# Optimization experiments

Hardware: AMD Instinct MI355X
Metric: run time of the kernel (lower is better)

The kernel has to match this reference:

```python
import jax, jax.numpy as jnp
import numpy as np

N = 100000        # nodes
E = 1600000       # edges (before self-loops)
IN_CH = 256       # input features
HEADS = 8         # conv1 heads; per-head dim also 8 (GATConv(in, heads, heads=heads))
HID = 8
NCLASS = 64
SLOPE = 0.2       # PyG leaky_relu negative slope


def _gat_conv(x, edge_index, W, att_src, att_dst, bias, heads, ch, concat):
    """PyG GATConv (eval mode): gather -> leaky_relu score -> segment softmax -> scatter."""
    n = x.shape[0]
    src, dst = edge_index[0], edge_index[1]
    h = (x @ W).reshape(n, heads, ch)                      # [N, H, C]
    a_src = jnp.einsum('nhc,hc->nh', h, att_src)           # [N, H]
    a_dst = jnp.einsum('nhc,hc->nh', h, att_dst)
    alpha = jax.nn.leaky_relu(a_src[src] + a_dst[dst], SLOPE)  # [E, H]
    # segment softmax over destination node
    amax = jax.ops.segment_max(alpha, dst, num_segments=n)     # [N, H]
    ex = jnp.exp(alpha - amax[dst])
    denom = jax.ops.segment_sum(ex, dst, num_segments=n)
    coef = ex / (denom[dst] + 1e-16)                           # [E, H]
    out = jax.ops.segment_sum(coef[:, :, None] * h[src], dst, num_segments=n)  # [N, H, C]
    if concat:
        out = out.reshape(n, heads * ch)
    else:
        out = out.mean(axis=1)
    return out + bias


def _add_self_loops(edge_index, n):
    loop = jnp.arange(n, dtype=edge_index.dtype)
    return jnp.concatenate([edge_index, jnp.stack([loop, loop])], axis=1)


def setup_inputs() -> dict:
    key = jax.random.key(0)
    ks = jax.random.split(key, 10)
    g = lambda k, shp, s: (jax.random.normal(k, shp, jnp.float32) * s)
    return {
        'x': jax.random.normal(ks[0], (N, IN_CH), jnp.float32),
        'edge_index': jax.random.randint(ks[1], (2, E), 0, N, dtype=jnp.int64),
        'W1': g(ks[2], (IN_CH, HEADS * HID), 1.0 / np.sqrt(IN_CH)),
        'att_src1': g(ks[3], (HEADS, HID), 0.3),
        'att_dst1': g(ks[4], (HEADS, HID), 0.3),
        'b1': jnp.zeros((HEADS * HID,), jnp.float32),
        'W2': g(ks[5], (HEADS * HID, NCLASS), 1.0 / np.sqrt(HEADS * HID)),
        'att_src2': g(ks[6], (1, NCLASS), 0.3),
        'att_dst2': g(ks[7], (1, NCLASS), 0.3),
        'b2': jnp.zeros((NCLASS,), jnp.float32),
    }


def reference(x, edge_index, W1, att_src1, att_dst1, b1, W2, att_src2, att_dst2, b2):
    ei = _add_self_loops(edge_index, x.shape[0])
    h = jax.nn.elu(_gat_conv(x, ei, W1, att_src1, att_dst1, b1, HEADS, HID, True))
    # dropout is a no-op in eval mode
    h = _gat_conv(h, ei, W2, att_src2, att_dst2, b2, 1, NCLASS, False)
    return jax.nn.log_softmax(h, axis=-1)
```

## Files before the change

### kernel.cpp

```cpp
#include <hip/hip_runtime.h>
#include <hip/hip_bf16.h>

#define LRELU_SLOPE 0.2f
#define CH2 6144
#define NBUK 256
#define BCAP 9728

typedef unsigned int uint;
typedef unsigned short ushort;
typedef short bt8 __attribute__((ext_vector_type(8)));
typedef float fx4 __attribute__((ext_vector_type(4)));

__device__ __forceinline__ float lrelu(float a) {
    return a > 0.f ? a : LRELU_SLOPE * a;
}
__device__ __forceinline__ ushort f2bf(float f) {
    uint u = __float_as_uint(f);
    return (ushort)((u + 0x7FFF + ((u >> 16) & 1)) >> 16);
}
__device__ __forceinline__ float bf2f(ushort h) {
    return __uint_as_float(((uint)h) << 16);
}

__global__ __launch_bounds__(256) void prep_wt(
    const float* __restrict__ W1, const float* __restrict__ W2,
    ushort* __restrict__ WT1, ushort* __restrict__ WT2)
{
    int idx = blockIdx.x * 256 + threadIdx.x;
    if (idx < 64 * 256) {
        int c = idx >> 8, k = idx & 255;
        WT1[idx] = f2bf(W1[k * 64 + c]);
    }
    int i2 = idx - 64 * 256;
    if (i2 >= 0 && i2 < 64 * 64) {
        int c = i2 >> 6, k = i2 & 63;
        WT2[i2] = f2bf(W2[k * 64 + c]);
    }
}

template<int K, bool INF32>
__global__ __launch_bounds__(256) void gemm_mfma(
    const void* __restrict__ Xv, const ushort* __restrict__ WT,
    ushort* __restrict__ OUT, int nrows)
{
    constexpr int LDW = K + 8;
    __shared__ ushort wt_l[64 * LDW];
    __shared__ ushort a_l[64 * 40];
    const int t = threadIdx.x;
    const int base = blockIdx.x * 64;

    for (int idx = t * 8; idx < 64 * K; idx += 256 * 8) {
        int r = idx / K, c = idx % K;
        *(uint4*)&wt_l[r * LDW + c] = *(const uint4*)&WT[idx];
    }
    __syncthreads();

    const int w = t >> 6, l = t & 63;
    const int frow = l & 15;
    const int kof = (l >> 4) * 8;
    fx4 acc[4] = {};

    for (int k0 = 0; k0 < K; k0 += 32) {
        if constexpr (INF32) {
            const float* X = (const float*)Xv;
            #pragma unroll
            for (int half = 0; half < 2; ++half) {
                int r = (t >> 3) + 32 * half;
                int kq = (t & 7) * 4;
                int gr = base + r;
                float4 v = make_float4(0.f, 0.f, 0.f, 0.f);
                if (gr < nrows) v = *(const float4*)(X + (size_t)gr * K + k0 + kq);
                ushort4 o;
                o.x = f2bf(v.x); o.y = f2bf(v.y); o.z = f2bf(v.z); o.w = f2bf(v.w);
                *(ushort4*)&a_l[r * 40 + kq] = o;
            }
        } else {
            const ushort* X = (const ushort*)Xv;
            int r = t >> 2;
            int kq = (t & 3) * 8;
            int gr = base + r;
            uint4 v = make_uint4(0, 0, 0, 0);
            if (gr < nrows) v = *(const uint4*)(X + (size_t)gr * K + k0 + kq);
            *(uint4*)&a_l[r * 40 + kq] = v;
        }
        __syncthreads();
        bt8 af = *(const bt8*)&a_l[(16 * w + frow) * 40 + kof];
        #pragma unroll
        for (int g = 0; g < 4; ++g) {
            bt8 bf = *(const bt8*)&wt_l[(16 * g + frow) * LDW + k0 + kof];
            acc[g] = __builtin_amdgcn_mfma_f32_16x16x32_bf16(af, bf, acc[g], 0, 0, 0);
        }
        __syncthreads();
    }

    const int orow0 = base + 16 * w + (l >> 4) * 4;
    const int ocol = l & 15;
    #pragma unroll
    for (int g = 0; g < 4; ++g) {
        #pragma unroll
        for (int r4 = 0; r4 < 4; ++r4) {
            int gr = orow0 + r4;
            if (gr < nrows) OUT[(size_t)gr * 64 + 16 * g + ocol] = f2bf(acc[g][r4]);
        }
    }
}

__global__ __launch_bounds__(256) void node_att_h8(
    const ushort* __restrict__ H, const float* __restrict__ att_s,
    const float* __restrict__ att_d,
    float* __restrict__ a_src, float* __restrict__ a_dst, int n)
{
    int node = blockIdx.x * 4 + (threadIdx.x >> 6);
    if (node >= n) return;
    int lane = threadIdx.x & 63;
    float h = bf2f(H[(size_t)node * 64 + lane]);
    float ps = h * att_s[lane];
    float pd = h * att_d[lane];
    #pragma unroll
    for (int off = 1; off < 8; off <<= 1) {
        ps += __shfl_xor(ps, off, 64);
        pd += __shfl_xor(pd, off, 64);
    }
    if ((lane & 7) == 0) {
        a_src[(size_t)node * 8 + (lane >> 3)] = ps;
        a_dst[(size_t)node * 8 + (lane >> 3)] = pd;
    }
}

__global__ __launch_bounds__(256) void node_att_h1(
    const ushort* __restrict__ H, const float* __restrict__ att_s,
    const float* __restrict__ att_d,
    float* __restrict__ a_src, float* __restrict__ a_dst, int n)
{
    int node = blockIdx.x * 4 + (threadIdx.x >> 6);
    if (node >= n) return;
    int lane = threadIdx.x & 63;
    float h = bf2f(H[(size_t)node * 64 + lane]);
    float ps = h * att_s[lane];
    float pd = h * att_d[lane];
    #pragma unroll
    for (int off = 1; off < 64; off <<= 1) {
        ps += __shfl_xor(ps, off, 64);
        pd += __shfl_xor(pd, off, 64);
    }
    if (lane == 0) { a_src[node] = ps; a_dst[node] = pd; }
}

__global__ void init_pcur(int* __restrict__ pcur)
{
    int t = threadIdx.x;
    if (t < NBUK) pcur[t] = t * BCAP;
}

__global__ __launch_bounds__(1024) void partition_pairs(
    const int* __restrict__ ei, int E_, int ET,
    int* __restrict__ pcur, uint* __restrict__ pairs)
{
    __shared__ int lcnt[NBUK], lsc[NBUK], lplace[NBUK], gpos[NBUK];
    const int t = threadIdx.x;
    const int base = blockIdx.x * CH2;
    const int total = min(CH2, ET - base);
    if (total <= 0) return;

    if (t < NBUK) lcnt[t] = 0;
    __syncthreads();

    uint pp[6]; int pk[6];
    #pragma unroll
    for (int i = 0; i < 6; ++i) {
        int idx = t + i * 1024;
        pk[i] = -1;
        if (idx < total) {
            int e = base + idx;
            int s, d;
            if (e < E_) { s = ei[e]; d = ei[E_ + e]; } else { s = d = e - E_; }
            pk[i] = d >> 9;
            pp[i] = (uint)s | ((uint)(d & 511) << 17);
            atomicAdd(&lcnt[pk[i]], 1);
        }
    }
    __syncthreads();

    if (t < NBUK) lsc[t] = lcnt[t];
    __syncthreads();
    for (int off = 1; off < NBUK; off <<= 1) {
        int add = 0;
        if (t < NBUK && t >= off) add = lsc[t - off];
        __syncthreads();
        if (t < NBUK) lsc[t] += add;
        __syncthreads();
    }
    if (t < NBUK) {
        int excl = lsc[t] - lcnt[t];
        lplace[t] = excl;
        int c = lcnt[t];
        gpos[t] = c ? (atomicAdd(&pcur[t], c) - excl) : 0;
    }
    __syncthreads();

    #pragma unroll
    for (int i = 0; i < 6; ++i) {
        if (pk[i] >= 0) {
            int slot = atomicAdd(&lplace[pk[i]], 1);
            pairs[gpos[pk[i]] + slot] = pp[i];
        }
    }
}

__global__ __launch_bounds__(256) void bucket_scan(
    const int* __restrict__ pcur, int* __restrict__ boff, int nbuk_used)
{
    __shared__ int sm[NBUK];
    int t = threadIdx.x;
    int v = (t < nbuk_used) ? (pcur[t] - t * BCAP) : 0;
    sm[t] = v; __syncthreads();
    for (int off = 1; off < NBUK; off <<= 1) {
        int add = (t >= off) ? sm[t - off] : 0;
        __syncthreads();
        sm[t] += add;
        __syncthreads();
    }
    boff[t] = sm[t] - v;
}

__global__ __launch_bounds__(1024) void phase2_build(
    const uint* __restrict__ pairs, const int* __restrict__ pcur,
    const int* __restrict__ boff,
    int* __restrict__ rp, int* __restrict__ ssrc, int n)
{
    __shared__ int hist[512], cur[512];
    const int k = blockIdx.x;
    const int t = threadIdx.x;
    const int beg = k * BCAP;
    const int cnt = pcur[k] - beg;
    const int bbase = boff[k];
    const int dbase = k << 9;

    if (t < 512) hist[t] = 0;
    __syncthreads();

    for (int i = t; i < cnt; i += 1024)
        atomicAdd(&hist[pairs[beg + i] >> 17], 1);
    __syncthreads();

    int c0 = (t < 512) ? hist[t] : 0;
    for (int off = 1; off < 512; off <<= 1) {
        int add = 0;
        if (t < 512 && t >= off) add = hist[t - off];
        __syncthreads();
        if (t < 512) hist[t] += add;
        __syncthreads();
    }
    if (t < 512) {
        int node = dbase + t;
        if (node < n) rp[node] = bbase + hist[t];
        cur[t] = hist[t] - c0;
    }
    __syncthreads();

    for (int i = t; i < cnt; i += 1024) {
        uint p = pairs[beg + i];
        int j = p >> 17;
        int pos = bbase + atomicAdd(&cur[j], 1);
        ssrc[pos] = (int)(p & 0x1FFFF);
    }
}

__global__ __launch_bounds__(256) void gather_h8(
    const int* __restrict__ rp, const int* __restrict__ ssrc,
    const float* __restrict__ a_src, const float* __restrict__ a_dst,
    const ushort* __restrict__ HB, const float* __restrict__ bias,
    ushort* __restrict__ HACT, int n)
{
    int node = blockIdx.x * 32 + (threadIdx.x >> 3);
    if (node >= n) return;
    int ol = threadIdx.x & 7;
    int end = rp[node];
    int start = node ? rp[node - 1] : 0;
    float adh = a_dst[(size_t)node * 8 + ol];
    float acc[8] = {};
    float dsum = 0.f;

    for (int i0 = start; i0 < end; i0 += 8) {
        int cnt = min(8, end - i0);
        int sv = (ol < cnt) ? ssrc[i0 + ol] : 0;
        #pragma unroll
        for (int j = 0; j < 8; ++j) {
            int sj = __shfl(sv, j, 8);
            float a = a_src[(size_t)sj * 8 + ol] + adh;
            a = a > 0.f ? a : LRELU_SLOPE * a;
            float e = __expf(a);
            e = (j < cnt) ? e : 0.f;
            dsum += e;
            uint4 hv = *(const uint4*)(HB + (size_t)sj * 64 + ol * 8);
            acc[0] += e * bf2f((ushort)(hv.x & 0xffff));
            acc[1] += e * bf2f((ushort)(hv.x >> 16));
            acc[2] += e * bf2f((ushort)(hv.y & 0xffff));
            acc[3] += e * bf2f((ushort)(hv.y >> 16));
            acc[4] += e * bf2f((ushort)(hv.z & 0xffff));
            acc[5] += e * bf2f((ushort)(hv.z >> 16));
            acc[6] += e * bf2f((ushort)(hv.w & 0xffff));
            acc[7] += e * bf2f((ushort)(hv.w >> 16));
        }
    }
    float inv = 1.f / (dsum + 1e-16f);
    float4 b0 = *(const float4*)(bias + ol * 8);
    float4 b1 = *(const float4*)(bias + ol * 8 + 4);
    float v[8];
    v[0] = acc[0] * inv + b0.x; v[1] = acc[1] * inv + b0.y;
    v[2] = acc[2] * inv + b0.z; v[3] = acc[3] * inv + b0.w;
    v[4] = acc[4] * inv + b1.x; v[5] = acc[5] * inv + b1.y;
    v[6] = acc[6] * inv + b1.z; v[7] = acc[7] * inv + b1.w;
    #pragma unroll
    for (int c = 0; c < 8; ++c) v[c] = v[c] > 0.f ? v[c] : expm1f(v[c]);
    uint4 o;
    o.x = (uint)f2bf(v[0]) | ((uint)f2bf(v[1]) << 16);
    o.y = (uint)f2bf(v[2]) | ((uint)f2bf(v[3]) << 16);
    o.z = (uint)f2bf(v[4]) | ((uint)f2bf(v[5]) << 16);
    o.w = (uint)f2bf(v[6]) | ((uint)f2bf(v[7]) << 16);
    *(uint4*)(HACT + (size_t)node * 64 + ol * 8) = o;
}

__global__ __launch_bounds__(256) void gather_h1_lsm(
    const int* __restrict__ rp, const int* __restrict__ ssrc,
    const float* __restrict__ a_src, const float* __restrict__ a_dst,
    const ushort* __restrict__ HB, const float* __restrict__ bias,
    float* __restrict__ OUT, int n)
{
    int node = blockIdx.x * 32 + (threadIdx.x >> 3);
    if (node >= n) return;
    int ol = threadIdx.x & 7;
    int end = rp[node];
    int start = node ? rp[node - 1] : 0;
    float ad = a_dst[node];
    float acc[8] = {};
    float dsum = 0.f;

    for (int i0 = start; i0 < end; i0 += 8) {
        int cnt = min(8, end - i0);
        int sv = (ol < cnt) ? ssrc[i0 + ol] : 0;
        #pragma unroll
        for (int j = 0; j < 8; ++j) {
            int sj = __shfl(sv, j, 8);
            float a = a_src[sj] + ad;
            a = a > 0.f ? a : LRELU_SLOPE * a;
            float e = __expf(a);
            e = (j < cnt) ? e : 0.f;
            dsum += e;
            uint4 hv = *(const uint4*)(HB + (size_t)sj * 64 + ol * 8);
            acc[0] += e * bf2f((ushort)(hv.x & 0xffff));
            acc[1] += e * bf2f((ushort)(hv.x >> 16));
            acc[2] += e * bf2f((ushort)(hv.y & 0xffff));
            acc[3] += e * bf2f((ushort)(hv.y >> 16));
            acc[4] += e * bf2f((ushort)(hv.z & 0xffff));
            acc[5] += e * bf2f((ushort)(hv.z >> 16));
            acc[6] += e * bf2f((ushort)(hv.w & 0xffff));
            acc[7] += e * bf2f((ushort)(hv.w >> 16));
        }
    }
    float inv = 1.f / (dsum + 1e-16f);
    float4 b0 = *(const float4*)(bias + ol * 8);
    float4 b1 = *(const float4*)(bias + ol * 8 + 4);
    float v[8];
    v[0] = acc[0] * inv + b0.x; v[1] = acc[1] * inv + b0.y;
    v[2] = acc[2] * inv + b0.z; v[3] = acc[3] * inv + b0.w;
    v[4] = acc[4] * inv + b1.x; v[5] = acc[5] * inv + b1.y;
    v[6] = acc[6] * inv + b1.z; v[7] = acc[7] * inv + b1.w;

    float m = v[0];
    #pragma unroll
    for (int c = 1; c < 8; ++c) m = fmaxf(m, v[c]);
    m = fmaxf(m, __shfl_xor(m, 1, 8));
    m = fmaxf(m, __shfl_xor(m, 2, 8));
    m = fmaxf(m, __shfl_xor(m, 4, 8));
    float s = 0.f;
    #pragma unroll
    for (int c = 0; c < 8; ++c) s += __expf(v[c] - m);
    s += __shfl_xor(s, 1, 8);
    s += __shfl_xor(s, 2, 8);
    s += __shfl_xor(s, 4, 8);
    float lse = m + __logf(s);
    float4 o0 = make_float4(v[0] - lse, v[1] - lse, v[2] - lse, v[3] - lse);
    float4 o1 = make_float4(v[4] - lse, v[5] - lse, v[6] - lse, v[7] - lse);
    *(float4*)(OUT + (size_t)node * 64 + ol * 8) = o0;
    *(float4*)(OUT + (size_t)node * 64 + ol * 8 + 4) = o1;
}

extern "C" void kernel_launch(void* const* d_in, const int* in_sizes, int n_in,
                              void* d_out, int out_size, void* d_ws, size_t ws_size,
                              hipStream_t stream)
{
    const float* x    = (const float*)d_in[0];
    const int*   ei   = (const int*)d_in[1];
    const float* W1   = (const float*)d_in[2];
    const float* as1w = (const float*)d_in[3];
    const float* ad1w = (const float*)d_in[4];
    const float* b1   = (const float*)d_in[5];
    const float* W2   = (const float*)d_in[6];
    const float* as2w = (const float*)d_in[7];
    const float* ad2w = (const float*)d_in[8];
    const float* b2   = (const float*)d_in[9];
    float* out = (float*)d_out;

    const int n  = in_sizes[0] / 256;
    const int E_ = in_sizes[1] / 2;
    const int ET = E_ + n;
    const int NBUKU = (n + 511) >> 9;

    char* wsb = (char*)d_ws;
    ushort* HACT = (ushort*)wsb;
    uint*   pairs= (uint*)wsb;
    ushort* HB   = HACT + (size_t)n * 64;
    float*  a_s1 = (float*)(HB + (size_t)n * 64);
    float*  a_d1 = a_s1 + (size_t)n * 8;
    float*  a_s2 = a_d1 + (size_t)n * 8;
    float*  a_d2 = a_s2 + n;
    int*    rp   = (int*)(a_d2 + n);
    int*    pcur = rp + n;
    int*    boff = pcur + NBUK;
    int*    ssrc = boff + NBUK;
    ushort* WT1  = (ushort*)(ssrc + ET);
    ushort* WT2  = WT1 + 64 * 256;

    const int gemm_grid = (n + 63) / 64;
    const int natt_grid = (n + 3) / 4;
    const int gath_grid = (n + 31) / 32;
    const int part_grid = (ET + CH2 - 1) / CH2;

    prep_wt<<<80, 256, 0, stream>>>(W1, W2, WT1, WT2);
    init_pcur<<<1, NBUK, 0, stream>>>(pcur);
    partition_pairs<<<part_grid, 1024, 0, stream>>>(ei, E_, ET, pcur, pairs);
    bucket_scan<<<1, NBUK, 0, stream>>>(pcur, boff, NBUKU);
    phase2_build<<<NBUKU, 1024, 0, stream>>>(pairs, pcur, boff, rp, ssrc, n);

    gemm_mfma<256, true><<<gemm_grid, 256, 0, stream>>>(x, WT1, HB, n);
    node_att_h8<<<natt_grid, 256, 0, stream>>>(HB, as1w, ad1w, a_s1, a_d1, n);
    gather_h8<<<gath_grid, 256, 0, stream>>>(rp, ssrc, a_s1, a_d1, HB, b1, HACT, n);

    gemm_mfma<64, false><<<gemm_grid, 256, 0, stream>>>(HACT, WT2, HB, n);
    node_att_h1<<<natt_grid, 256, 0, stream>>>(HB, as2w, ad2w, a_s2, a_d2, n);
    gather_h1_lsm<<<gath_grid, 256, 0, stream>>>(rp, ssrc, a_s2, a_d2, HB, b2, out, n);
}
```

Measured before the change: 189.6 us.

## Fuse partition with GEMM1, attention into GEMM epilogue, bucket scan into build

Several kernels are merged. Edge partitioning and the first GEMM now run as a single heterogeneous launch at 256-thread blocks over smaller chunks. The per-node attention dot products move into the GEMM epilogue using warp shuffles, the bucket scan is folded into phase2_build, and pcur init is folded into weight prep. The GEMM now reads weights directly from global memory instead of staging them in LDS, and the gather loops process 16 edges per iteration to expose more memory parallelism. The aim is fewer launches and fewer HB re-reads, at the cost of uncached weight reads and a redundant scan in every build block.

```diff
diff --git a/kernel.cpp b/kernel.cpp
--- a/kernel.cpp
+++ b/kernel.cpp
@@ -2,18 +2,15 @@
 #include <hip/hip_bf16.h>
 
 #define LRELU_SLOPE 0.2f
-#define CH2 6144
 #define NBUK 256
 #define BCAP 9728
+#define CH1 1536
 
 typedef unsigned int uint;
 typedef unsigned short ushort;
 typedef short bt8 __attribute__((ext_vector_type(8)));
 typedef float fx4 __attribute__((ext_vector_type(4)));
 
-__device__ __forceinline__ float lrelu(float a) {
-    return a > 0.f ? a : LRELU_SLOPE * a;
-}
 __device__ __forceinline__ ushort f2bf(float f) {
     uint u = __float_as_uint(f);
     return (ushort)((u + 0x7FFF + ((u >> 16) & 1)) >> 16);
@@ -22,11 +19,23 @@
     return __uint_as_float(((uint)h) << 16);
 }
 
-__global__ __launch_bounds__(256) void prep_wt(
+#define ACC8(e, hv) \
+    acc[0] += (e) * bf2f((ushort)((hv).x & 0xffff)); \
+    acc[1] += (e) * bf2f((ushort)((hv).x >> 16));    \
+    acc[2] += (e) * bf2f((ushort)((hv).y & 0xffff)); \
+    acc[3] += (e) * bf2f((ushort)((hv).y >> 16));    \
+    acc[4] += (e) * bf2f((ushort)((hv).z & 0xffff)); \
+    acc[5] += (e) * bf2f((ushort)((hv).z >> 16));    \
+    acc[6] += (e) * bf2f((ushort)((hv).w & 0xffff)); \
+    acc[7] += (e) * bf2f((ushort)((hv).w >> 16));
+
+__global__ __launch_bounds__(256) void prep_init(
     const float* __restrict__ W1, const float* __restrict__ W2,
-    ushort* __restrict__ WT1, ushort* __restrict__ WT2)
-{
-    int idx = blockIdx.x * 256 + threadIdx.x;
+    ushort* __restrict__ WT1, ushort* __restrict__ WT2, int* __restrict__ pcur)
+{
+    int t = threadIdx.x;
+    int idx = blockIdx.x * 256 + t;
+    if (blockIdx.x == 0) pcur[t] = t * BCAP;
     if (idx < 64 * 256) {
         int c = idx >> 8, k = idx & 255;
         WT1[idx] = f2bf(W1[k * 64 + c]);
@@ -38,23 +47,69 @@
     }
 }
 
-template<int K, bool INF32>
-__global__ __launch_bounds__(256) void gemm_mfma(
-    const void* __restrict__ Xv, const ushort* __restrict__ WT,
-    ushort* __restrict__ OUT, int nrows)
-{
-    constexpr int LDW = K + 8;
-    __shared__ ushort wt_l[64 * LDW];
-    __shared__ ushort a_l[64 * 40];
+__device__ __forceinline__ void partition_body(
+    int bid, const int* __restrict__ ei, int E_, int ET,
+    int* __restrict__ pcur, uint* __restrict__ pairs,
+    int* lcnt, int* lsc, int* lplace, int* gpos)
+{
     const int t = threadIdx.x;
-    const int base = blockIdx.x * 64;
-
-    for (int idx = t * 8; idx < 64 * K; idx += 256 * 8) {
-        int r = idx / K, c = idx % K;
-        *(uint4*)&wt_l[r * LDW + c] = *(const uint4*)&WT[idx];
-    }
-    __syncthreads();
-
+    const int base = bid * CH1;
+    const int total = min(CH1, ET - base);
+    if (total <= 0) return;
+
+    lcnt[t] = 0;
+    __syncthreads();
+
+    uint pp[6]; int pk[6];
+    #pragma unroll
+    for (int i = 0; i < 6; ++i) {
+        int idx = t + i * 256;
+        pk[i] = -1;
+        if (idx < total) {
+            int e = base + idx;
+            int s, d;
+            if (e < E_) { s = ei[e]; d = ei[E_ + e]; } else { s = d = e - E_; }
+            pk[i] = d >> 9;
+            pp[i] = (uint)s | ((uint)(d & 511) << 17);
+            atomicAdd(&lcnt[pk[i]], 1);
+        }
+    }
+    __syncthreads();
+
+    lsc[t] = lcnt[t];
+    __syncthreads();
+    for (int off = 1; off < NBUK; off <<= 1) {
+        int add = (t >= off) ? lsc[t - off] : 0;
+        __syncthreads();
+        lsc[t] += add;
+        __syncthreads();
+    }
+    {
+        int excl = lsc[t] - lcnt[t];
+        lplace[t] = excl;
+        int c = lcnt[t];
+        gpos[t] = c ? (atomicAdd(&pcur[t], c) - excl) : 0;
+    }
+    __syncthreads();
+
+    #pragma unroll
+    for (int i = 0; i < 6; ++i) {
+        if (pk[i] >= 0) {
+            int slot = atomicAdd(&lplace[pk[i]], 1);
+            pairs[gpos[pk[i]] + slot] = pp[i];
+        }
+    }
+}
+
+template<int K, bool INF32, int HEADS>
+__device__ __forceinline__ void gemm_body(
+    int bid, const void* __restrict__ Xv, const ushort* __restrict__ WT,
+    ushort* __restrict__ OUT, float* __restrict__ a_src, float* __restrict__ a_dst,
+    const float* __restrict__ att_s, const float* __restrict__ att_d,
+    int nrows, ushort* a_l)
+{
+    const int t = threadIdx.x;
+    const int base = bid * 64;
     const int w = t >> 6, l = t & 63;
     const int frow = l & 15;
     const int kof = (l >> 4) * 8;
@@ -76,8 +131,7 @@
             }
         } else {
             const ushort* X = (const ushort*)Xv;
-            int r = t >> 2;
-            int kq = (t & 3) * 8;
+            int r = t >> 2, kq = (t & 3) * 8;
             int gr = base + r;
             uint4 v = make_uint4(0, 0, 0, 0);
             if (gr < nrows) v = *(const uint4*)(X + (size_t)gr * K + k0 + kq);
@@ -87,7 +141,7 @@
         bt8 af = *(const bt8*)&a_l[(16 * w + frow) * 40 + kof];
         #pragma unroll
         for (int g = 0; g < 4; ++g) {
-            bt8 bf = *(const bt8*)&wt_l[(16 * g + frow) * LDW + k0 + kof];
+            bt8 bf = *(const bt8*)&WT[(size_t)(16 * g + frow) * K + k0 + kof];
             acc[g] = __builtin_amdgcn_mfma_f32_16x16x32_bf16(af, bf, acc[g], 0, 0, 0);
         }
         __syncthreads();
@@ -103,141 +157,99 @@
             if (gr < nrows) OUT[(size_t)gr * 64 + 16 * g + ocol] = f2bf(acc[g][r4]);
         }
     }
-}
-
-__global__ __launch_bounds__(256) void node_att_h8(
-    const ushort* __restrict__ H, const float* __restrict__ att_s,
-    const float* __restrict__ att_d,
-    float* __restrict__ a_src, float* __restrict__ a_dst, int n)
-{
-    int node = blockIdx.x * 4 + (threadIdx.x >> 6);
-    if (node >= n) return;
-    int lane = threadIdx.x & 63;
-    float h = bf2f(H[(size_t)node * 64 + lane]);
-    float ps = h * att_s[lane];
-    float pd = h * att_d[lane];
-    #pragma unroll
-    for (int off = 1; off < 8; off <<= 1) {
-        ps += __shfl_xor(ps, off, 64);
-        pd += __shfl_xor(pd, off, 64);
-    }
-    if ((lane & 7) == 0) {
-        a_src[(size_t)node * 8 + (lane >> 3)] = ps;
-        a_dst[(size_t)node * 8 + (lane >> 3)] = pd;
-    }
-}
-
-__global__ __launch_bounds__(256) void node_att_h1(
-    const ushort* __restrict__ H, const float* __restrict__ att_s,
-    const float* __restrict__ att_d,
-    float* __restrict__ a_src, float* __restrict__ a_dst, int n)
-{
-    int node = blockIdx.x * 4 + (threadIdx.x >> 6);
-    if (node >= n) return;
-    int lane = threadIdx.x & 63;
-    float h = bf2f(H[(size_t)node * 64 + lane]);
-    float ps = h * att_s[lane];
-    float pd = h * att_d[lane];
-    #pragma unroll
-    for (int off = 1; off < 64; off <<= 1) {
-        ps += __shfl_xor(ps, off, 64);
-        pd += __shfl_xor(pd, off, 64);
-    }
-    if (lane == 0) { a_src[node] = ps; a_dst[node] = pd; }
-}
-
-__global__ void init_pcur(int* __restrict__ pcur)
-{
-    int t = threadIdx.x;
-    if (t < NBUK) pcur[t] = t * BCAP;
-}
-
-__global__ __launch_bounds__(1024) void partition_pairs(
-    const int* __restrict__ ei, int E_, int ET,
-    int* __restrict__ pcur, uint* __restrict__ pairs)
+
+    float as_c[4], ad_c[4];
+    #pragma unroll
+    for (int g = 0; g < 4; ++g) {
+        as_c[g] = att_s[16 * g + ocol];
+        ad_c[g] = att_d[16 * g + ocol];
+    }
+    if constexpr (HEADS == 8) {
+        #pragma unroll
+        for (int r4 = 0; r4 < 4; ++r4) {
+            int gr = orow0 + r4;
+            #pragma unroll
+            for (int g = 0; g < 4; ++g) {
+                float ps = acc[g][r4] * as_c[g];
+                float pd = acc[g][r4] * ad_c[g];
+                ps += __shfl_xor(ps, 1, 64); pd += __shfl_xor(pd, 1, 64);
+                ps += __shfl_xor(ps, 2, 64); pd += __shfl_xor(pd, 2, 64);
+                ps += __shfl_xor(ps, 4, 64); pd += __shfl_xor(pd, 4, 64);
+                if ((l & 7) == 0 && gr < nrows) {
+                    int head = 2 * g + ((l >> 3) & 1);
+                    a_src[(size_t)gr * 8 + head] = ps;
+                    a_dst[(size_t)gr * 8 + head] = pd;
+                }
+            }
+        }
+    } else {
+        #pragma unroll
+        for (int r4 = 0; r4 < 4; ++r4) {
+            int gr = orow0 + r4;
+            float ps = 0.f, pd = 0.f;
+            #pragma unroll
+            for (int g = 0; g < 4; ++g) {
+                ps += acc[g][r4] * as_c[g];
+                pd += acc[g][r4] * ad_c[g];
+            }
+            ps += __shfl_xor(ps, 1, 64); pd += __shfl_xor(pd, 1, 64);
+            ps += __shfl_xor(ps, 2, 64); pd += __shfl_xor(pd, 2, 64);
+            ps += __shfl_xor(ps, 4, 64); pd += __shfl_xor(pd, 4, 64);
+            ps += __shfl_xor(ps, 8, 64); pd += __shfl_xor(pd, 8, 64);
+            if ((l & 15) == 0 && gr < nrows) {
+                a_src[gr] = ps;
+                a_dst[gr] = pd;
+            }
+        }
+    }
+}
+
+__global__ __launch_bounds__(256) void part_gemm1(
+    const int* __restrict__ ei, int E_, int ET, int part_grid,
+    int* __restrict__ pcur, uint* __restrict__ pairs,
+    const float* __restrict__ x, const ushort* __restrict__ WT1,
+    ushort* __restrict__ HB, float* __restrict__ a_s1, float* __restrict__ a_d1,
+    const float* __restrict__ att_s, const float* __restrict__ att_d, int n)
 {
     __shared__ int lcnt[NBUK], lsc[NBUK], lplace[NBUK], gpos[NBUK];
-    const int t = threadIdx.x;
-    const int base = blockIdx.x * CH2;
-    const int total = min(CH2, ET - base);
-    if (total <= 0) return;
-
-    if (t < NBUK) lcnt[t] = 0;
-    __syncthreads();
-
-    uint pp[6]; int pk[6];
-    #pragma unroll
-    for (int i = 0; i < 6; ++i) {
-        int idx = t + i * 1024;
-        pk[i] = -1;
-        if (idx < total) {
-            int e = base + idx;
-            int s, d;
-            if (e < E_) { s = ei[e]; d = ei[E_ + e]; } else { s = d = e - E_; }
-            pk[i] = d >> 9;
-            pp[i] = (uint)s | ((uint)(d & 511) << 17);
-            atomicAdd(&lcnt[pk[i]], 1);
-        }
-    }
-    __syncthreads();
-
-    if (t < NBUK) lsc[t] = lcnt[t];
-    __syncthreads();
-    for (int off = 1; off < NBUK; off <<= 1) {
-        int add = 0;
-        if (t < NBUK && t >= off) add = lsc[t - off];
-        __syncthreads();
-        if (t < NBUK) lsc[t] += add;
-        __syncthreads();
-    }
-    if (t < NBUK) {
-        int excl = lsc[t] - lcnt[t];
-        lplace[t] = excl;
-        int c = lcnt[t];
-        gpos[t] = c ? (atomicAdd(&pcur[t], c) - excl) : 0;
-    }
-    __syncthreads();
-
-    #pragma unroll
-    for (int i = 0; i < 6; ++i) {
-        if (pk[i] >= 0) {
-            int slot = atomicAdd(&lplace[pk[i]], 1);
-            pairs[gpos[pk[i]] + slot] = pp[i];
-        }
-    }
-}
-
-__global__ __launch_bounds__(256) void bucket_scan(
-    const int* __restrict__ pcur, int* __restrict__ boff, int nbuk_used)
-{
-    __shared__ int sm[NBUK];
-    int t = threadIdx.x;
-    int v = (t < nbuk_used) ? (pcur[t] - t * BCAP) : 0;
-    sm[t] = v; __syncthreads();
-    for (int off = 1; off < NBUK; off <<= 1) {
-        int add = (t >= off) ? sm[t - off] : 0;
-        __syncthreads();
-        sm[t] += add;
-        __syncthreads();
-    }
-    boff[t] = sm[t] - v;
+    __shared__ ushort a_l[64 * 40];
+    if ((int)blockIdx.x < part_grid)
+        partition_body(blockIdx.x, ei, E_, ET, pcur, pairs, lcnt, lsc, lplace, gpos);
+    else
+        gemm_body<256, true, 8>(blockIdx.x - part_grid, x, WT1, HB,
+                                a_s1, a_d1, att_s, att_d, n, a_l);
+}
+
+__global__ __launch_bounds__(256) void gemm2_att(
+    const ushort* __restrict__ HACT, const ushort* __restrict__ WT2,
+    ushort* __restrict__ HB, float* __restrict__ a_s2, float* __restrict__ a_d2,
+    const float* __restrict__ att_s, const float* __restrict__ att_d, int n)
+{
+    __shared__ ushort a_l[64 * 40];
+    gemm_body<64, false, 1>(blockIdx.x, HACT, WT2, HB, a_s2, a_d2, att_s, att_d, n, a_l);
 }
 
 __global__ __launch_bounds__(1024) void phase2_build(
     const uint* __restrict__ pairs, const int* __restrict__ pcur,
-    const int* __restrict__ boff,
-    int* __restrict__ rp, int* __restrict__ ssrc, int n)
-{
-    __shared__ int hist[512], cur[512];
+    int* __restrict__ rp, int* __restrict__ ssrc, int n, int nbuk_used)
+{
+    __shared__ int hist[512], cur[512], psc[NBUK];
     const int k = blockIdx.x;
     const int t = threadIdx.x;
     const int beg = k * BCAP;
     const int cnt = pcur[k] - beg;
-    const int bbase = boff[k];
     const int dbase = k << 9;
 
     if (t < 512) hist[t] = 0;
-    __syncthreads();
+    if (t < NBUK) psc[t] = (t < nbuk_used) ? (pcur[t] - t * BCAP) : 0;
+    __syncthreads();
+    for (int off = 1; off < NBUK; off <<= 1) {
+        int add = (t < NBUK && t >= off) ? psc[t - off] : 0;
+        __syncthreads();
+        if (t < NBUK) psc[t] += add;
+        __syncthreads();
+    }
+    const int bbase = k ? psc[k - 1] : 0;
 
     for (int i = t; i < cnt; i += 1024)
         atomicAdd(&hist[pairs[beg + i] >> 17], 1);
@@ -245,8 +257,7 @@
 
     int c0 = (t < 512) ? hist[t] : 0;
     for (int off = 1; off < 512; off <<= 1) {
-        int add = 0;
-        if (t < 512 && t >= off) add = hist[t - off];
+        int add = (t < 512 && t >= off) ? hist[t - off] : 0;
         __syncthreads();
         if (t < 512) hist[t] += add;
         __syncthreads();
@@ -281,7 +292,27 @@
     float acc[8] = {};
     float dsum = 0.f;
 
-    for (int i0 = start; i0 < end; i0 += 8) {
+    int i0 = start;
+    for (; i0 + 16 <= end; i0 += 16) {
+        int svA = ssrc[i0 + ol];
+        int svB = ssrc[i0 + 8 + ol];
+        #pragma unroll
+        for (int j = 0; j < 8; ++j) {
+            int sjA = __shfl(svA, j, 8);
+            float aA = a_src[(size_t)sjA * 8 + ol] + adh;
+            aA = aA > 0.f ? aA : LRELU_SLOPE * aA;
+            float eA = __expf(aA);
+            uint4 hvA = *(const uint4*)(HB + (size_t)sjA * 64 + ol * 8);
+            dsum += eA; ACC8(eA, hvA);
+            int sjB = __shfl(svB, j, 8);
+            float aB = a_src[(size_t)sjB * 8 + ol] + adh;
+            aB = aB > 0.f ? aB : LRELU_SLOPE * aB;
+            float eB = __expf(aB);
+            uint4 hvB = *(const uint4*)(HB + (size_t)sjB * 64 + ol * 8);
+            dsum += eB; ACC8(eB, hvB);
+        }
+    }
+    for (; i0 < end; i0 += 8) {
         int cnt = min(8, end - i0);
         int sv = (ol < cnt) ? ssrc[i0 + ol] : 0;
         #pragma unroll
@@ -291,16 +322,8 @@
             a = a > 0.f ? a : LRELU_SLOPE * a;
             float e = __expf(a);
             e = (j < cnt) ? e : 0.f;
-            dsum += e;
             uint4 hv = *(const uint4*)(HB + (size_t)sj * 64 + ol * 8);
-            acc[0] += e * bf2f((ushort)(hv.x & 0xffff));
-            acc[1] += e * bf2f((ushort)(hv.x >> 16));
-            acc[2] += e * bf2f((ushort)(hv.y & 0xffff));
-            acc[3] += e * bf2f((ushort)(hv.y >> 16));
-            acc[4] += e * bf2f((ushort)(hv.z & 0xffff));
-            acc[5] += e * bf2f((ushort)(hv.z >> 16));
-            acc[6] += e * bf2f((ushort)(hv.w & 0xffff));
-            acc[7] += e * bf2f((ushort)(hv.w >> 16));
+            dsum += e; ACC8(e, hv);
         }
     }
     float inv = 1.f / (dsum + 1e-16f);
@@ -336,7 +359,27 @@
     float acc[8] = {};
     float dsum = 0.f;
 
-    for (int i0 = start; i0 < end; i0 += 8) {
+    int i0 = start;
+    for (; i0 + 16 <= end; i0 += 16) {
+        int svA = ssrc[i0 + ol];
+        int svB = ssrc[i0 + 8 + ol];
+        #pragma unroll
+        for (int j = 0; j < 8; ++j) {
+            int sjA = __shfl(svA, j, 8);
+            float aA = a_src[sjA] + ad;
+            aA = aA > 0.f ? aA : LRELU_SLOPE * aA;
+            float eA = __expf(aA);
+            uint4 hvA = *(const uint4*)(HB + (size_t)sjA * 64 + ol * 8);
+            dsum += eA; ACC8(eA, hvA);
+            int sjB = __shfl(svB, j, 8);
+            float aB = a_src[sjB] + ad;
+            aB = aB > 0.f ? aB : LRELU_SLOPE * aB;
+            float eB = __expf(aB);
+            uint4 hvB = *(const uint4*)(HB + (size_t)sjB * 64 + ol * 8);
+            dsum += eB; ACC8(eB, hvB);
+        }
+    }
+    for (; i0 < end; i0 += 8) {
         int cnt = min(8, end - i0);
         int sv = (ol < cnt) ? ssrc[i0 + ol] : 0;
         #pragma unroll
@@ -346,16 +389,8 @@
             a = a > 0.f ? a : LRELU_SLOPE * a;
             float e = __expf(a);
             e = (j < cnt) ? e : 0.f;
-            dsum += e;
             uint4 hv = *(const uint4*)(HB + (size_t)sj * 64 + ol * 8);
-            acc[0] += e * bf2f((ushort)(hv.x & 0xffff));
-            acc[1] += e * bf2f((ushort)(hv.x >> 16));
-            acc[2] += e * bf2f((ushort)(hv.y & 0xffff));
-            acc[3] += e * bf2f((ushort)(hv.y >> 16));
-            acc[4] += e * bf2f((ushort)(hv.z & 0xffff));
-            acc[5] += e * bf2f((ushort)(hv.z >> 16));
-            acc[6] += e * bf2f((ushort)(hv.w & 0xffff));
-            acc[7] += e * bf2f((ushort)(hv.w >> 16));
+            dsum += e; ACC8(e, hv);
         }
     }
     float inv = 1.f / (dsum + 1e-16f);
@@ -408,36 +443,28 @@
     const int NBUKU = (n + 511) >> 9;
 
     char* wsb = (char*)d_ws;
-    ushort* HACT = (ushort*)wsb;
     uint*   pairs= (uint*)wsb;
-    ushort* HB   = HACT + (size_t)n * 64;
-    float*  a_s1 = (float*)(HB + (size_t)n * 64);
+    ushort* HB   = (ushort*)(pairs + (size_t)NBUK*BCAP);
+    ushort* HACT = HB + (size_t)n * 64;
+    float*  a_s1 = (float*)(HACT + (size_t)n * 64);
     float*  a_d1 = a_s1 + (size_t)n * 8;
     float*  a_s2 = a_d1 + (size_t)n * 8;
     float*  a_d2 = a_s2 + n;
     int*    rp   = (int*)(a_d2 + n);
     int*    pcur = rp + n;
-    int*    boff = pcur + NBUK;
-    int*    ssrc = boff + NBUK;
+    int*    ssrc = pcur + NBUK;
     ushort* WT1  = (ushort*)(ssrc + ET);
     ushort* WT2  = WT1 + 64 * 256;
 
     const int gemm_grid = (n + 63) / 64;
-    const int natt_grid = (n + 3) / 4;
     const int gath_grid = (n + 31) / 32;
-    const int part_grid = (ET + CH2 - 1) / CH2;
-
-    prep_wt<<<80, 256, 0, stream>>>(W1, W2, WT1, WT2);
-    init_pcur<<<1, NBUK, 0, stream>>>(pcur);
-    partition_pairs<<<part_grid, 1024, 0, stream>>>(ei, E_, ET, pcur, pairs);
-    bucket_scan<<<1, NBUK, 0, stream>>>(pcur, boff, NBUKU);
-    phase2_build<<<NBUKU, 1024, 0, stream>>>(pairs, pcur, boff, rp, ssrc, n);
-
-    gemm_mfma<256, true><<<gemm_grid, 256, 0, stream>>>(x, WT1, HB, n);
-    node_att_h8<<<natt_grid, 256, 0, stream>>>(HB, as1w, ad1w, a_s1, a_d1, n);
+    const int part_grid = (ET + CH1 - 1) / CH1;
+
+    prep_init<<<80, 256, 0, stream>>>(W1, W2, WT1, WT2, pcur);
+    part_gemm1<<<part_grid + gemm_grid, 256, 0, stream>>>(
+        ei, E_, ET, part_grid, pcur, pairs, x, WT1, HB, a_s1, a_d1, as1w, ad1w, n);
+    phase2_build<<<NBUKU, 1024, 0, stream>>>(pairs, pcur, rp, ssrc, n, NBUKU);
     gather_h8<<<gath_grid, 256, 0, stream>>>(rp, ssrc, a_s1, a_d1, HB, b1, HACT, n);
-
-    gemm_mfma<64, false><<<gemm_grid, 256, 0, stream>>>(HACT, WT2, HB, n);
-    node_att_h1<<<natt_grid, 256, 0, stream>>>(HB, as2w, ad2w, a_s2, a_d2, n);
+    gemm2_att<<<gemm_grid, 256, 0, stream>>>(HACT, WT2, HB, a_s2, a_d2, as2w, ad2w, n);
     gather_h1_lsm<<<gath_grid, 256, 0, stream>>>(rp, ssrc, a_s2, a_d2, HB, b2, out, n);
 }
```

Result: slower. 209.8 us (+10.6%).
